# Optimization experiments

Measured on AMD Instinct MI355X. Metric: run time of the kernel, lower is better.

## Reference

```python
import jax, jax.numpy as jnp
import numpy as np

EPS = 1e-5

def _bn(x, gamma, beta):
    # x: [B, N, C]; training-mode BatchNorm1d over (B, N)
    mu = jnp.mean(x, axis=(0, 1))
    var = jnp.var(x, axis=(0, 1))
    return (x - mu) * jax.lax.rsqrt(var + EPS) * gamma + beta


def setup_inputs() -> dict:
    key = jax.random.key(0)
    ks = jax.random.split(key, 32)
    B, N = 16, 8192
    enc_dim, mem_dim = 1024, 1024
    feat_dim = enc_dim + mem_dim  # 2048
    n_points = 2048
    s = 0.02
    d = {
        'partial': jax.random.normal(ks[0], (B, N, 3), jnp.float32),
        # first_conv: Conv1d(3,128,1) + BN(128) + ReLU + Conv1d(128,256,1)
        'W1': jax.random.normal(ks[1], (128, 3), jnp.float32) * s,
        'b1': jnp.zeros((128,), jnp.float32),
        'g1': jnp.ones((128,), jnp.float32),
        'be1': jnp.zeros((128,), jnp.float32),
        'W2': jax.random.normal(ks[2], (256, 128), jnp.float32) * s,
        'b2': jnp.zeros((256,), jnp.float32),
        # second_conv: Conv1d(512,512,1) + BN(512) + ReLU + Conv1d(512,enc_dim,1)
        'W3': jax.random.normal(ks[3], (512, 512), jnp.float32) * s,
        'b3': jnp.zeros((512,), jnp.float32),
        'g2': jnp.ones((512,), jnp.float32),
        'be2': jnp.zeros((512,), jnp.float32),
        'W4': jax.random.normal(ks[4], (enc_dim, 512), jnp.float32) * s,
        'b4': jnp.zeros((enc_dim,), jnp.float32),
        # MemoryModule gates: Linear(enc_dim, mem_dim) x4 + memory param
        'Wf': jax.random.normal(ks[5], (mem_dim, enc_dim), jnp.float32) * s,
        'bf': jnp.zeros((mem_dim,), jnp.float32),
        'Wi': jax.random.normal(ks[6], (mem_dim, enc_dim), jnp.float32) * s,
        'bi': jnp.zeros((mem_dim,), jnp.float32),
        'Wo': jax.random.normal(ks[7], (mem_dim, enc_dim), jnp.float32) * s,
        'bo': jnp.zeros((mem_dim,), jnp.float32),
        'Wc': jax.random.normal(ks[8], (mem_dim, enc_dim), jnp.float32) * s,
        'bc': jnp.zeros((mem_dim,), jnp.float32),
        'mem': jax.random.normal(ks[9], (1, mem_dim), jnp.float32),
        # Decoder MLP: feat_dim->2048->2048->2048->3*n_points
        'D1w': jax.random.normal(ks[10], (2048, feat_dim), jnp.float32) * s,
        'D1b': jnp.zeros((2048,), jnp.float32),
        'D2w': jax.random.normal(ks[11], (2048, 2048), jnp.float32) * s,
        'D2b': jnp.zeros((2048,), jnp.float32),
        'D3w': jax.random.normal(ks[12], (2048, 2048), jnp.float32) * s,
        'D3b': jnp.zeros((2048,), jnp.float32),
        'D4w': jax.random.normal(ks[13], (3 * n_points, 2048), jnp.float32) * s,
        'D4b': jnp.zeros((3 * n_points,), jnp.float32),
    }
    return d


def reference(partial, W1, b1, g1, be1, W2, b2, W3, b3, g2, be2, W4, b4,
              Wf, bf, Wi, bi, Wo, bo, Wc, bc, mem,
              D1w, D1b, D2w, D2b, D3w, D3b, D4w, D4b):
    B, N, _ = partial.shape
    # --- Encoder first_conv (pointwise convs == per-point linear) ---
    f = jnp.einsum('bnc,dc->bnd', partial, W1) + b1          # [B,N,128]
    f = jax.nn.relu(_bn(f, g1, be1))
    f = jnp.einsum('bnc,dc->bnd', f, W2) + b2                # [B,N,256]
    fg = jnp.max(f, axis=1, keepdims=True)                   # [B,1,256]
    f = jnp.concatenate([jnp.broadcast_to(fg, (B, N, 256)), f], axis=-1)  # [B,N,512]
    # --- second_conv ---
    f = jnp.einsum('bnc,dc->bnd', f, W3) + b3                # [B,N,512]
    f = jax.nn.relu(_bn(f, g2, be2))
    f = jnp.einsum('bnc,dc->bnd', f, W4) + b4                # [B,N,enc_dim]
    feat_global = jnp.max(f, axis=1)                         # [B,enc_dim]
    # --- MemoryModule (flag=False: memory not updated) ---
    fgate = jax.nn.sigmoid(feat_global @ Wf.T + bf)
    igate = jax.nn.sigmoid(feat_global @ Wi.T + bi)
    ogate = jax.nn.sigmoid(feat_global @ Wo.T + bo)
    cand = jnp.tanh(feat_global @ Wc.T + bc)
    mem_b = jnp.broadcast_to(mem, fgate.shape)
    h = ogate * jnp.tanh(fgate * mem_b + igate * cand)       # [B,mem_dim]
    feat = jnp.concatenate([feat_global, h], axis=1)         # [B,feat_dim]
    # --- Decoder MLP ---
    z = jax.nn.relu(feat @ D1w.T + D1b)
    z = jax.nn.relu(z @ D2w.T + D2b)
    z = jax.nn.relu(z @ D3w.T + D3b)
    z = z @ D4w.T + D4b                                      # [B, 3*n_points]
    return z.reshape(B, -1, 3)
```

## Files before the change

### kernel.cpp

```cpp
#include <hip/hip_runtime.h>
#include <hip/hip_bf16.h>

typedef __bf16 v8bf __attribute__((ext_vector_type(8)));
typedef float  v4f  __attribute__((ext_vector_type(4)));

#define NPTS (16*8192)
#define RPB  8192

__device__ __forceinline__ unsigned fenc(float x){
    unsigned u = __float_as_uint(x);
    return (u & 0x80000000u) ? ~u : (u | 0x80000000u);
}
__device__ __forceinline__ float fdec(unsigned u){
    return __uint_as_float((u & 0x80000000u) ? (u ^ 0x80000000u) : ~u);
}

__device__ __forceinline__ v8bf bn_relu8(v8bf v, float4 s0, float4 s1, float4 h0, float4 h1){
    v8bf r;
    r[0] = (__bf16)fmaxf(fmaf((float)v[0], s0.x, h0.x), 0.f);
    r[1] = (__bf16)fmaxf(fmaf((float)v[1], s0.y, h0.y), 0.f);
    r[2] = (__bf16)fmaxf(fmaf((float)v[2], s0.z, h0.z), 0.f);
    r[3] = (__bf16)fmaxf(fmaf((float)v[3], s0.w, h0.w), 0.f);
    r[4] = (__bf16)fmaxf(fmaf((float)v[4], s1.x, h1.x), 0.f);
    r[5] = (__bf16)fmaxf(fmaf((float)v[5], s1.y, h1.y), 0.f);
    r[6] = (__bf16)fmaxf(fmaf((float)v[6], s1.z, h1.z), 0.f);
    r[7] = (__bf16)fmaxf(fmaf((float)v[7], s1.w, h1.w), 0.f);
    return r;
}

__global__ __launch_bounds__(256) void stats1_k(const float* __restrict__ P,
        const float* __restrict__ W1, const float* __restrict__ b1,
        float* __restrict__ gsum, float* __restrict__ gsumsq)
{
    int tid = threadIdx.x;
    int c = tid & 127, half = tid >> 7;
    float w0 = W1[c*3+0], w1 = W1[c*3+1], w2 = W1[c*3+2], bb = b1[c];
    float s = 0.f, s2 = 0.f;
    int base = blockIdx.x * 512 + half;
    for (int i = 0; i < 256; ++i) {
        int p = base + i*2;
        float x = P[p*3+0], y = P[p*3+1], z = P[p*3+2];
        float v = fmaf(w0,x, fmaf(w1,y, fmaf(w2,z, bb)));
        s += v; s2 = fmaf(v,v,s2);
    }
    __shared__ float ls[256], lq[256];
    ls[tid] = s; lq[tid] = s2;
    __syncthreads();
    if (half == 0) {
        atomicAdd(&gsum[c],   s  + ls[tid+128]);
        atomicAdd(&gsumsq[c], s2 + lq[tid+128]);
    }
}

__global__ void finalize_k(const float* __restrict__ gsum, const float* __restrict__ gsumsq,
        const float* __restrict__ gamma, const float* __restrict__ beta,
        float* __restrict__ scale, float* __restrict__ shift, int C, float invn)
{
    int c = blockIdx.x*blockDim.x + threadIdx.x;
    if (c >= C) return;
    float m   = gsum[c]*invn;
    float var = fmaxf(gsumsq[c]*invn - m*m, 0.f);
    float rs  = rsqrtf(var + 1e-5f);
    float sc  = gamma[c]*rs;
    scale[c] = sc;
    shift[c] = beta[c] - m*sc;
}

__global__ __launch_bounds__(256) void apply1_k(const float* __restrict__ P,
        const float* __restrict__ W1, const float* __restrict__ b1,
        const float* __restrict__ sc, const float* __restrict__ sh,
        __bf16* __restrict__ out)
{
    int tid = threadIdx.x;
    int c = tid & 127, ph = tid >> 7;
    float w0 = W1[c*3+0], w1 = W1[c*3+1], w2 = W1[c*3+2], bb = b1[c];
    float a = sc[c], b_ = sh[c];
    int base = blockIdx.x * 16 + ph;
    #pragma unroll
    for (int i = 0; i < 8; ++i) {
        int p = base + i*2;
        float x = P[p*3+0], y = P[p*3+1], z = P[p*3+2];
        float v = fmaf(w0,x, fmaf(w1,y, fmaf(w2,z, bb)));
        v = fmaxf(fmaf(v, a, b_), 0.f);
        out[(size_t)p*128 + c] = (__bf16)v;
    }
}

__global__ void cvt_k(const float* __restrict__ src, __bf16* __restrict__ dst,
                      int rows, int cols, int sstride, int coff)
{
    int i = blockIdx.x*256 + threadIdx.x;
    if (i >= rows*cols) return;
    int r = i / cols, c = i - r*cols;
    dst[i] = (__bf16)src[(size_t)r*sstride + coff + c];
}

template<bool STORE, bool DOMAX, bool STATS, bool BNA, int LOGNB>
__global__ __launch_bounds__(256, 2) void gemm_k(
        const __bf16* __restrict__ A, const __bf16* __restrict__ Bw,
        int K, int Nw,
        const float* __restrict__ bias, int bias_bstride,
        __bf16* __restrict__ Cout, unsigned* __restrict__ maxenc,
        float* __restrict__ gsum, float* __restrict__ gsq,
        const float* __restrict__ scA, const float* __restrict__ shA)
{
    __shared__ __bf16 As[128*64];
    __shared__ __bf16 Bs[128*64];
    __shared__ float lstat[2][2][128];

    const int tid  = threadIdx.x;
    const int lane = tid & 63;
    const int wave = tid >> 6;
    const int wr = wave >> 1, wc = wave & 1;

    const int nwg   = (int)gridDim.x;
    const int chunk = nwg >> 3;
    const int bi    = (int)blockIdx.x;
    const int li    = (bi & 7) * chunk + (bi >> 3);
    const int m0    = (li >> LOGNB) * 128;
    const int n0    = (li & ((1 << LOGNB) - 1)) * 128;

    const int srow = tid >> 3, sslot = tid & 7;

    v4f acc[4][4];
    #pragma unroll
    for (int i=0;i<4;i++)
      #pragma unroll
      for (int j=0;j<4;j++) acc[i][j] = (v4f)(0.0f);

    v8bf ra[4], rb[4];
    auto loadAB = [&](int kb){
        float4 s0{}, s1{}, h0{}, h1{};
        if constexpr (BNA) {
            int kk = kb + sslot*8;
            s0 = *(const float4*)(scA + kk);
            s1 = *(const float4*)(scA + kk + 4);
            h0 = *(const float4*)(shA + kk);
            h1 = *(const float4*)(shA + kk + 4);
        }
        #pragma unroll
        for (int i=0;i<4;i++){
            int r = i*32 + srow;
            v8bf v = *(const v8bf*)(A + (size_t)(m0+r)*K + kb + sslot*8);
            if constexpr (BNA) v = bn_relu8(v, s0, s1, h0, h1);
            ra[i] = v;
            rb[i] = *(const v8bf*)(Bw + (size_t)(n0+r)*K + kb + sslot*8);
        }
    };

    loadAB(0);

    for (int k0 = 0; k0 < K; k0 += 64) {
        __syncthreads();
        #pragma unroll
        for (int i=0;i<4;i++){
            int r = i*32 + srow;
            int p = sslot ^ (r & 7);
            *(v8bf*)(&As[r*64 + p*8]) = ra[i];
            *(v8bf*)(&Bs[r*64 + p*8]) = rb[i];
        }
        __syncthreads();
        if (k0 + 64 < K) loadAB(k0 + 64);
        #pragma unroll
        for (int kk = 0; kk < 2; ++kk) {
            v8bf af[4], bfr[4];
            #pragma unroll
            for (int i=0;i<4;i++){
                int arow = wr*64 + i*16 + (lane & 15);
                int slog = kk*4 + (lane >> 4);
                af[i]  = *(const v8bf*)(&As[arow*64 + ((slog ^ (arow & 7))<<3)]);
                int brow = wc*64 + i*16 + (lane & 15);
                bfr[i] = *(const v8bf*)(&Bs[brow*64 + ((slog ^ (brow & 7))<<3)]);
            }
            #pragma unroll
            for (int i=0;i<4;i++)
              #pragma unroll
              for (int j=0;j<4;j++)
                acc[i][j] = __builtin_amdgcn_mfma_f32_16x16x32_bf16(af[i], bfr[j], acc[i][j], 0,0,0);
        }
    }

    const int b = m0 / RPB;
    const float* brow_ = bias + (size_t)b * bias_bstride;
    float colmax[4], csum[4], csq[4];
    #pragma unroll
    for (int j=0;j<4;j++){ colmax[j] = -3.402823466e38f; csum[j]=0.f; csq[j]=0.f; }

    #pragma unroll
    for (int i=0;i<4;i++){
        int rbase = m0 + wr*64 + i*16 + ((lane>>4)<<2);
        #pragma unroll
        for (int j=0;j<4;j++){
            int col = n0 + wc*64 + j*16 + (lane & 15);
            float bv = brow_[col];
            #pragma unroll
            for (int q=0;q<4;q++){
                float v = acc[i][j][q] + bv;
                if constexpr (STORE) Cout[(size_t)(rbase+q)*Nw + col] = (__bf16)v;
                if constexpr (DOMAX) colmax[j] = fmaxf(colmax[j], v);
                if constexpr (STATS) { csum[j] += v; csq[j] = fmaf(v,v,csq[j]); }
            }
        }
    }
    if constexpr (DOMAX) {
        #pragma unroll
        for (int j=0;j<4;j++){
            float v = colmax[j];
            v = fmaxf(v, __shfl_xor(v, 16));
            v = fmaxf(v, __shfl_xor(v, 32));
            if (lane < 16) {
                int col = n0 + wc*64 + j*16 + lane;
                atomicMax(&maxenc[(size_t)b*Nw + col], fenc(v));
            }
        }
    }
    if constexpr (STATS) {
        #pragma unroll
        for (int j=0;j<4;j++){
            float s = csum[j], q = csq[j];
            s += __shfl_xor(s, 16); s += __shfl_xor(s, 32);
            q += __shfl_xor(q, 16); q += __shfl_xor(q, 32);
            if (lane < 16) {
                int c = wc*64 + j*16 + lane;
                lstat[0][wr][c] = s;
                lstat[1][wr][c] = q;
            }
        }
        __syncthreads();
        if (tid < 128) {
            float s = lstat[0][0][tid] + lstat[0][1][tid];
            float q = lstat[1][0][tid] + lstat[1][1][tid];
            atomicAdd(&gsum[n0 + tid], s);
            atomicAdd(&gsq [n0 + tid], q);
        }
    }
}

__global__ __launch_bounds__(256) void bias3_k(const unsigned* __restrict__ fge,
        const float* __restrict__ W3, const float* __restrict__ b3,
        float* __restrict__ bias3)
{
    int b = blockIdx.x, tid = threadIdx.x;
    __shared__ float fg[256];
    fg[tid] = fdec(fge[b*256 + tid]);
    __syncthreads();
    for (int d = tid; d < 512; d += 256) {
        const float* wrow = W3 + (size_t)d*512;
        float s = b3[d];
        for (int c = 0; c < 256; c += 4) {
            s = fmaf(fg[c+0], wrow[c+0], s);
            s = fmaf(fg[c+1], wrow[c+1], s);
            s = fmaf(fg[c+2], wrow[c+2], s);
            s = fmaf(fg[c+3], wrow[c+3], s);
        }
        bias3[b*512 + d] = s;
    }
}

__global__ void decode_k(const unsigned* __restrict__ enc, float* __restrict__ feat)
{
    int i = blockIdx.x*256 + threadIdx.x;
    int b = i >> 10, c = i & 1023;
    feat[(size_t)b*2048 + c] = fdec(enc[i]);
}

__global__ __launch_bounds__(256) void gates_k(
        const float* __restrict__ Wf, const float* __restrict__ bfv,
        const float* __restrict__ Wi, const float* __restrict__ biv,
        const float* __restrict__ Wo, const float* __restrict__ bov,
        const float* __restrict__ Wc, const float* __restrict__ bcv,
        const float* __restrict__ memv, float* __restrict__ feat)
{
    int tid = threadIdx.x;
    int b = tid & 15;
    int j = blockIdx.x*16 + (tid >> 4);
    const float* x  = feat + (size_t)b*2048;
    const float* rf = Wf + (size_t)j*1024;
    const float* ri = Wi + (size_t)j*1024;
    const float* ro = Wo + (size_t)j*1024;
    const float* rc = Wc + (size_t)j*1024;
    float sf = bfv[j], si = biv[j], so = bov[j], scn = bcv[j];
    for (int c = 0; c < 1024; c += 4) {
        float4 xv = *(const float4*)(x + c);
        float4 a  = *(const float4*)(rf + c);
        sf = fmaf(xv.x,a.x, fmaf(xv.y,a.y, fmaf(xv.z,a.z, fmaf(xv.w,a.w, sf))));
        float4 bq = *(const float4*)(ri + c);
        si = fmaf(xv.x,bq.x, fmaf(xv.y,bq.y, fmaf(xv.z,bq.z, fmaf(xv.w,bq.w, si))));
        float4 cq = *(const float4*)(ro + c);
        so = fmaf(xv.x,cq.x, fmaf(xv.y,cq.y, fmaf(xv.z,cq.z, fmaf(xv.w,cq.w, so))));
        float4 dq = *(const float4*)(rc + c);
        scn= fmaf(xv.x,dq.x, fmaf(xv.y,dq.y, fmaf(xv.z,dq.z, fmaf(xv.w,dq.w, scn))));
    }
    float fg = 1.f/(1.f + expf(-sf));
    float ig = 1.f/(1.f + expf(-si));
    float og = 1.f/(1.f + expf(-so));
    float cd = tanhf(scn);
    float h  = og * tanhf(fmaf(fg, memv[j], ig*cd));
    feat[(size_t)b*2048 + 1024 + j] = h;
}

template<bool RELU>
__global__ __launch_bounds__(256) void dec_k(const float* __restrict__ in,
        const float* __restrict__ W, const float* __restrict__ bias,
        float* __restrict__ out, int N)
{
    __shared__ float xin[2048];
    int tid = threadIdx.x;
    int b    = (blockIdx.x*4) / N;
    int col0 = (blockIdx.x*4) % N;
    for (int k = tid; k < 2048; k += 256) xin[k] = in[(size_t)b*2048 + k];
    __syncthreads();
    int lane = tid & 63;
    int col  = col0 + (tid >> 6);
    const float* wrow = W + (size_t)col*2048;
    float s = 0.f;
    for (int k = lane*4; k < 2048; k += 256) {
        float4 wv = *(const float4*)(wrow + k);
        float4 xv = *(const float4*)(&xin[k]);
        s = fmaf(wv.x,xv.x, fmaf(wv.y,xv.y, fmaf(wv.z,xv.z, fmaf(wv.w,xv.w, s))));
    }
    #pragma unroll
    for (int off = 32; off; off >>= 1) s += __shfl_xor(s, off);
    if (lane == 0) {
        s += bias[col];
        if (RELU) s = fmaxf(s, 0.f);
        out[(size_t)b*N + col] = s;
    }
}

extern "C" void kernel_launch(void* const* d_in, const int* in_sizes, int n_in,
                              void* d_out, int out_size, void* d_ws, size_t ws_size,
                              hipStream_t stream)
{
    (void)in_sizes; (void)n_in; (void)out_size; (void)ws_size;
    const float* partial = (const float*)d_in[0];
    const float* W1 = (const float*)d_in[1];
    const float* b1 = (const float*)d_in[2];
    const float* g1 = (const float*)d_in[3];
    const float* be1= (const float*)d_in[4];
    const float* W2 = (const float*)d_in[5];
    const float* b2 = (const float*)d_in[6];
    const float* W3 = (const float*)d_in[7];
    const float* b3 = (const float*)d_in[8];
    const float* g2 = (const float*)d_in[9];
    const float* be2= (const float*)d_in[10];
    const float* W4 = (const float*)d_in[11];
    const float* b4 = (const float*)d_in[12];
    const float* Wf = (const float*)d_in[13];
    const float* bfv= (const float*)d_in[14];
    const float* Wi = (const float*)d_in[15];
    const float* biv= (const float*)d_in[16];
    const float* Wo = (const float*)d_in[17];
    const float* bov= (const float*)d_in[18];
    const float* Wc = (const float*)d_in[19];
    const float* bcv= (const float*)d_in[20];
    const float* memv=(const float*)d_in[21];
    const float* D1w= (const float*)d_in[22];
    const float* D1b= (const float*)d_in[23];
    const float* D2w= (const float*)d_in[24];
    const float* D2b= (const float*)d_in[25];
    const float* D3w= (const float*)d_in[26];
    const float* D3b= (const float*)d_in[27];
    const float* D4w= (const float*)d_in[28];
    const float* D4b= (const float*)d_in[29];

    char* w = (char*)d_ws;
    size_t off = 0;
    auto alloc = [&](size_t bytes) -> void* {
        void* p = w + off; off += (bytes + 255) & ~(size_t)255; return p;
    };
    __bf16* y1bn = (__bf16*)alloc((size_t)NPTS*128*2);
    __bf16* f2   = (__bf16*)alloc((size_t)NPTS*256*2);
    __bf16* y3   = (__bf16*)alloc((size_t)NPTS*512*2);
    __bf16* W2b  = (__bf16*)alloc(256*128*2);
    __bf16* W3bb = (__bf16*)alloc(512*256*2);
    __bf16* W4b  = (__bf16*)alloc(1024*512*2);
    char* accbase = (char*)(w + off);
    float* gsum1    = (float*)alloc(128*4);
    float* gsumsq1  = (float*)alloc(128*4);
    float* gsum3    = (float*)alloc(512*4);
    float* gsumsq3  = (float*)alloc(512*4);
    unsigned* fg_enc    = (unsigned*)alloc(16*256*4);
    unsigned* featg_enc = (unsigned*)alloc(16*1024*4);
    size_t accbytes = (size_t)((w + off) - accbase);
    float* scale1 = (float*)alloc(128*4);
    float* shift1 = (float*)alloc(128*4);
    float* scale3 = (float*)alloc(512*4);
    float* shift3 = (float*)alloc(512*4);
    float* bias3  = (float*)alloc(16*512*4);
    float* feat   = (float*)alloc(16*2048*4);
    float* z1     = (float*)alloc(16*2048*4);
    float* z2     = (float*)alloc(16*2048*4);
    float* z3     = (float*)alloc(16*2048*4);

    hipMemsetAsync(accbase, 0, accbytes, stream);

    cvt_k<<<dim3(128), 256, 0, stream>>>(W2, W2b, 256, 128, 128, 0);
    cvt_k<<<dim3(512), 256, 0, stream>>>(W3, W3bb, 512, 256, 512, 256);
    cvt_k<<<dim3(2048),256, 0, stream>>>(W4, W4b, 1024, 512, 512, 0);

    stats1_k<<<dim3(256), 256, 0, stream>>>(partial, W1, b1, gsum1, gsumsq1);
    finalize_k<<<dim3(1), 128, 0, stream>>>(gsum1, gsumsq1, g1, be1, scale1, shift1, 128, 1.f/NPTS);
    apply1_k<<<dim3(8192), 256, 0, stream>>>(partial, W1, b1, scale1, shift1, y1bn);

    gemm_k<true,true,false,false,1><<<dim3(2048), 256, 0, stream>>>(
        y1bn, W2b, 128, 256, b2, 0, f2, fg_enc, nullptr, nullptr, nullptr, nullptr);

    bias3_k<<<dim3(16), 256, 0, stream>>>(fg_enc, W3, b3, bias3);

    gemm_k<true,false,true,false,2><<<dim3(4096), 256, 0, stream>>>(
        f2, W3bb, 256, 512, bias3, 512, y3, nullptr, gsum3, gsumsq3, nullptr, nullptr);

    finalize_k<<<dim3(2), 256, 0, stream>>>(gsum3, gsumsq3, g2, be2, scale3, shift3, 512, 1.f/NPTS);

    gemm_k<false,true,false,true,3><<<dim3(8192), 256, 0, stream>>>(
        y3, W4b, 512, 1024, b4, 0, nullptr, featg_enc, nullptr, nullptr, scale3, shift3);

    decode_k<<<dim3(64), 256, 0, stream>>>(featg_enc, feat);
    gates_k<<<dim3(64), 256, 0, stream>>>(Wf,bfv, Wi,biv, Wo,bov, Wc,bcv, memv, feat);

    dec_k<true ><<<dim3(8192),  256, 0, stream>>>(feat, D1w, D1b, z1, 2048);
    dec_k<true ><<<dim3(8192),  256, 0, stream>>>(z1,   D2w, D2b, z2, 2048);
    dec_k<true ><<<dim3(8192),  256, 0, stream>>>(z2,   D3w, D3b, z3, 2048);
    dec_k<false><<<dim3(24576), 256, 0, stream>>>(z3,   D4w, D4b, (float*)d_out, 6144);
}
```

Before: 567.7 us.

## Add 256x256-tile 8-wave double-buffered GEMM for the two big pointwise convs

Adds a new GEMM kernel with 256x256 output tiles, 512 threads, a double-buffered LDS stage, phased MFMA issue with s_setprio, and BN scale/shift cached in LDS. It is used for the W3 and W4 convolutions in place of the 128x128 kernel, which raises data reuse per tile and overlaps global loads with compute. The original kernel is trimmed to the plain store/max path for W2. Larger tiles mean fewer workgroups and heavier register and LDS use per workgroup, which may limit occupancy.

```diff
diff --git a/kernel.cpp b/kernel.cpp
--- a/kernel.cpp
+++ b/kernel.cpp
@@ -95,31 +95,25 @@
     dst[i] = (__bf16)src[(size_t)r*sstride + coff + c];
 }
 
-template<bool STORE, bool DOMAX, bool STATS, bool BNA, int LOGNB>
+template<bool STORE, bool DOMAX, int LOGNB>
 __global__ __launch_bounds__(256, 2) void gemm_k(
         const __bf16* __restrict__ A, const __bf16* __restrict__ Bw,
         int K, int Nw,
         const float* __restrict__ bias, int bias_bstride,
-        __bf16* __restrict__ Cout, unsigned* __restrict__ maxenc,
-        float* __restrict__ gsum, float* __restrict__ gsq,
-        const float* __restrict__ scA, const float* __restrict__ shA)
+        __bf16* __restrict__ Cout, unsigned* __restrict__ maxenc)
 {
     __shared__ __bf16 As[128*64];
     __shared__ __bf16 Bs[128*64];
-    __shared__ float lstat[2][2][128];
-
     const int tid  = threadIdx.x;
     const int lane = tid & 63;
     const int wave = tid >> 6;
     const int wr = wave >> 1, wc = wave & 1;
-
     const int nwg   = (int)gridDim.x;
     const int chunk = nwg >> 3;
     const int bi    = (int)blockIdx.x;
     const int li    = (bi & 7) * chunk + (bi >> 3);
     const int m0    = (li >> LOGNB) * 128;
     const int n0    = (li & ((1 << LOGNB) - 1)) * 128;
-
     const int srow = tid >> 3, sslot = tid & 7;
 
     v4f acc[4][4];
@@ -129,26 +123,12 @@
       for (int j=0;j<4;j++) acc[i][j] = (v4f)(0.0f);
 
     v8bf ra[4], rb[4];
-    auto loadAB = [&](int kb){
-        float4 s0{}, s1{}, h0{}, h1{};
-        if constexpr (BNA) {
-            int kk = kb + sslot*8;
-            s0 = *(const float4*)(scA + kk);
-            s1 = *(const float4*)(scA + kk + 4);
-            h0 = *(const float4*)(shA + kk);
-            h1 = *(const float4*)(shA + kk + 4);
-        }
-        #pragma unroll
-        for (int i=0;i<4;i++){
-            int r = i*32 + srow;
-            v8bf v = *(const v8bf*)(A + (size_t)(m0+r)*K + kb + sslot*8);
-            if constexpr (BNA) v = bn_relu8(v, s0, s1, h0, h1);
-            ra[i] = v;
-            rb[i] = *(const v8bf*)(Bw + (size_t)(n0+r)*K + kb + sslot*8);
-        }
-    };
-
-    loadAB(0);
+    #pragma unroll
+    for (int i=0;i<4;i++){
+        int r = i*32 + srow;
+        ra[i] = *(const v8bf*)(A  + (size_t)(m0+r)*K + sslot*8);
+        rb[i] = *(const v8bf*)(Bw + (size_t)(n0+r)*K + sslot*8);
+    }
 
     for (int k0 = 0; k0 < K; k0 += 64) {
         __syncthreads();
@@ -160,7 +140,14 @@
             *(v8bf*)(&Bs[r*64 + p*8]) = rb[i];
         }
         __syncthreads();
-        if (k0 + 64 < K) loadAB(k0 + 64);
+        if (k0 + 64 < K) {
+            #pragma unroll
+            for (int i=0;i<4;i++){
+                int r = i*32 + srow;
+                ra[i] = *(const v8bf*)(A  + (size_t)(m0+r)*K + (k0+64) + sslot*8);
+                rb[i] = *(const v8bf*)(Bw + (size_t)(n0+r)*K + (k0+64) + sslot*8);
+            }
+        }
         #pragma unroll
         for (int kk = 0; kk < 2; ++kk) {
             v8bf af[4], bfr[4];
@@ -182,9 +169,9 @@
 
     const int b = m0 / RPB;
     const float* brow_ = bias + (size_t)b * bias_bstride;
-    float colmax[4], csum[4], csq[4];
-    #pragma unroll
-    for (int j=0;j<4;j++){ colmax[j] = -3.402823466e38f; csum[j]=0.f; csq[j]=0.f; }
+    float colmax[4];
+    #pragma unroll
+    for (int j=0;j<4;j++) colmax[j] = -3.402823466e38f;
 
     #pragma unroll
     for (int i=0;i<4;i++){
@@ -198,7 +185,6 @@
                 float v = acc[i][j][q] + bv;
                 if constexpr (STORE) Cout[(size_t)(rbase+q)*Nw + col] = (__bf16)v;
                 if constexpr (DOMAX) colmax[j] = fmaxf(colmax[j], v);
-                if constexpr (STATS) { csum[j] += v; csq[j] = fmaf(v,v,csq[j]); }
             }
         }
     }
@@ -214,7 +200,169 @@
             }
         }
     }
+}
+
+template<bool STORE, bool DOMAX, bool STATS, bool BNA, int LOGNB>
+__global__ __launch_bounds__(512, 2) void gemm8_k(
+        const __bf16* __restrict__ A, const __bf16* __restrict__ Bw,
+        int K, int Nw,
+        const float* __restrict__ bias, int bias_bstride,
+        __bf16* __restrict__ Cout, unsigned* __restrict__ maxenc,
+        float* __restrict__ gsum, float* __restrict__ gsq,
+        const float* __restrict__ scA, const float* __restrict__ shA)
+{
+    __shared__ __bf16 lds[2][2][256*64];
+    __shared__ float bnbuf[2][512];
+
+    const int tid  = threadIdx.x;
+    const int lane = tid & 63;
+    const int wave = tid >> 6;
+    const int wr = wave >> 2, wc = wave & 3;
+    const int nwg   = (int)gridDim.x;
+    const int chunk = nwg >> 3;
+    const int bi    = (int)blockIdx.x;
+    const int li    = (bi & 7) * chunk + (bi >> 3);
+    const int m0    = (li >> LOGNB) * 256;
+    const int n0    = (li & ((1 << LOGNB) - 1)) * 256;
+    const int srow = tid >> 3;
+    const int slot = tid & 7;
+
+    if constexpr (BNA) {
+        for (int c = tid; c < K; c += 512) {
+            bnbuf[0][c] = scA[c];
+            bnbuf[1][c] = shA[c];
+        }
+    }
+
+    v4f acc[8][4];
+    #pragma unroll
+    for (int i=0;i<8;i++)
+      #pragma unroll
+      for (int j=0;j<4;j++) acc[i][j] = (v4f)(0.0f);
+
+    v8bf ga[4], gb[4];
+    auto issue = [&](int kb){
+        #pragma unroll
+        for (int p=0;p<4;p++){
+            int r = p*64 + srow;
+            ga[p] = *(const v8bf*)(A  + (size_t)(m0+r)*K + kb + slot*8);
+            gb[p] = *(const v8bf*)(Bw + (size_t)(n0+r)*K + kb + slot*8);
+        }
+    };
+    auto wr_lds = [&](int buf, int kb){
+        float4 s0{}, s1{}, h0{}, h1{};
+        if constexpr (BNA) {
+            int kk = kb + slot*8;
+            s0 = *(const float4*)&bnbuf[0][kk];
+            s1 = *(const float4*)&bnbuf[0][kk+4];
+            h0 = *(const float4*)&bnbuf[1][kk];
+            h1 = *(const float4*)&bnbuf[1][kk+4];
+        }
+        #pragma unroll
+        for (int p=0;p<4;p++){
+            int r = p*64 + srow;
+            int sl = slot ^ (r & 7);
+            v8bf va = ga[p];
+            if constexpr (BNA) va = bn_relu8(va, s0, s1, h0, h1);
+            *(v8bf*)(&lds[buf][0][r*64 + sl*8]) = va;
+            *(v8bf*)(&lds[buf][1][r*64 + sl*8]) = gb[p];
+        }
+    };
+
+    if constexpr (BNA) __syncthreads();
+    issue(0);
+    wr_lds(0, 0);
+    issue(64);
+    __syncthreads();
+
+    const int nt = K >> 6;
+    for (int t = 0; t < nt; ++t) {
+        const __bf16* as_ = &lds[t & 1][0][0];
+        const __bf16* bs_ = &lds[t & 1][1][0];
+        v8bf bfr[4][2];
+        #pragma unroll
+        for (int ph = 0; ph < 4; ++ph) {
+            v8bf af[2][2];
+            if (ph == 0) {
+                #pragma unroll
+                for (int nf=0;nf<4;nf++)
+                  #pragma unroll
+                  for (int kk=0;kk<2;kk++){
+                    int brow = wc*64 + nf*16 + (lane & 15);
+                    int sg = kk*4 + (lane >> 4);
+                    bfr[nf][kk] = *(const v8bf*)(bs_ + brow*64 + ((sg ^ (brow & 7))<<3));
+                  }
+            }
+            #pragma unroll
+            for (int i=0;i<2;i++)
+              #pragma unroll
+              for (int kk=0;kk<2;kk++){
+                int arow = wr*128 + (ph*2+i)*16 + (lane & 15);
+                int sg = kk*4 + (lane >> 4);
+                af[i][kk] = *(const v8bf*)(as_ + arow*64 + ((sg ^ (arow & 7))<<3));
+              }
+            __builtin_amdgcn_s_barrier();
+            asm volatile("s_waitcnt lgkmcnt(0)" ::: "memory");
+            __builtin_amdgcn_sched_barrier(0);
+            __builtin_amdgcn_s_setprio(1);
+            #pragma unroll
+            for (int i=0;i<2;i++)
+              #pragma unroll
+              for (int nf=0;nf<4;nf++)
+                acc[ph*2+i][nf] = __builtin_amdgcn_mfma_f32_16x16x32_bf16(af[i][0], bfr[nf][0], acc[ph*2+i][nf], 0,0,0);
+            #pragma unroll
+            for (int i=0;i<2;i++)
+              #pragma unroll
+              for (int nf=0;nf<4;nf++)
+                acc[ph*2+i][nf] = __builtin_amdgcn_mfma_f32_16x16x32_bf16(af[i][1], bfr[nf][1], acc[ph*2+i][nf], 0,0,0);
+            __builtin_amdgcn_s_setprio(0);
+            if (ph < 3) {
+                __builtin_amdgcn_s_barrier();
+            } else {
+                __syncthreads();
+                if (t + 1 < nt) wr_lds((t+1) & 1, (t+1) << 6);
+                if (t + 2 < nt) issue((t+2) << 6);
+                __syncthreads();
+            }
+        }
+    }
+
+    const int b = m0 / RPB;
+    const float* brow_ = bias + (size_t)b * bias_bstride;
+    float colmax[4], csum[4], csq[4];
+    #pragma unroll
+    for (int j=0;j<4;j++){ colmax[j] = -3.402823466e38f; csum[j]=0.f; csq[j]=0.f; }
+
+    #pragma unroll
+    for (int i=0;i<8;i++){
+        int rbase = m0 + wr*128 + i*16 + ((lane>>4)<<2);
+        #pragma unroll
+        for (int j=0;j<4;j++){
+            int col = n0 + wc*64 + j*16 + (lane & 15);
+            float bv = brow_[col];
+            #pragma unroll
+            for (int q=0;q<4;q++){
+                float v = acc[i][j][q] + bv;
+                if constexpr (STORE) Cout[(size_t)(rbase+q)*Nw + col] = (__bf16)v;
+                if constexpr (DOMAX) colmax[j] = fmaxf(colmax[j], v);
+                if constexpr (STATS) { csum[j] += v; csq[j] = fmaf(v,v,csq[j]); }
+            }
+        }
+    }
+    if constexpr (DOMAX) {
+        #pragma unroll
+        for (int j=0;j<4;j++){
+            float v = colmax[j];
+            v = fmaxf(v, __shfl_xor(v, 16));
+            v = fmaxf(v, __shfl_xor(v, 32));
+            if (lane < 16) {
+                int col = n0 + wc*64 + j*16 + lane;
+                atomicMax(&maxenc[(size_t)b*Nw + col], fenc(v));
+            }
+        }
+    }
     if constexpr (STATS) {
+        float* lst = (float*)&lds[0][0][0];
         #pragma unroll
         for (int j=0;j<4;j++){
             float s = csum[j], q = csq[j];
@@ -222,14 +370,14 @@
             q += __shfl_xor(q, 16); q += __shfl_xor(q, 32);
             if (lane < 16) {
                 int c = wc*64 + j*16 + lane;
-                lstat[0][wr][c] = s;
-                lstat[1][wr][c] = q;
+                lst[(wr*2+0)*256 + c] = s;
+                lst[(wr*2+1)*256 + c] = q;
             }
         }
         __syncthreads();
-        if (tid < 128) {
-            float s = lstat[0][0][tid] + lstat[0][1][tid];
-            float q = lstat[1][0][tid] + lstat[1][1][tid];
+        if (tid < 256) {
+            float s = lst[0*256 + tid] + lst[2*256 + tid];
+            float q = lst[1*256 + tid] + lst[3*256 + tid];
             atomicAdd(&gsum[n0 + tid], s);
             atomicAdd(&gsq [n0 + tid], q);
         }
@@ -403,17 +551,17 @@
     finalize_k<<<dim3(1), 128, 0, stream>>>(gsum1, gsumsq1, g1, be1, scale1, shift1, 128, 1.f/NPTS);
     apply1_k<<<dim3(8192), 256, 0, stream>>>(partial, W1, b1, scale1, shift1, y1bn);
 
-    gemm_k<true,true,false,false,1><<<dim3(2048), 256, 0, stream>>>(
-        y1bn, W2b, 128, 256, b2, 0, f2, fg_enc, nullptr, nullptr, nullptr, nullptr);
+    gemm_k<true,true,1><<<dim3(2048), 256, 0, stream>>>(
+        y1bn, W2b, 128, 256, b2, 0, f2, fg_enc);
 
     bias3_k<<<dim3(16), 256, 0, stream>>>(fg_enc, W3, b3, bias3);
 
-    gemm_k<true,false,true,false,2><<<dim3(4096), 256, 0, stream>>>(
+    gemm8_k<true,false,true,false,1><<<dim3(1024), 512, 0, stream>>>(
         f2, W3bb, 256, 512, bias3, 512, y3, nullptr, gsum3, gsumsq3, nullptr, nullptr);
 
     finalize_k<<<dim3(2), 256, 0, stream>>>(gsum3, gsumsq3, g2, be2, scale3, shift3, 512, 1.f/NPTS);
 
-    gemm_k<false,true,false,true,3><<<dim3(8192), 256, 0, stream>>>(
+    gemm8_k<false,true,false,true,2><<<dim3(2048), 512, 0, stream>>>(
         y3, W4b, 512, 1024, b4, 0, nullptr, featg_enc, nullptr, nullptr, scale3, shift3);
 
     decode_k<<<dim3(64), 256, 0, stream>>>(featg_enc, feat);
```

Result: no change. 574.2 us (+1.1%).

## Batch decoder GEMV across all 16 samples to reuse each weight row

Applied to the files above, without the earlier changes.

The decoder MLP kernels previously read every weight row once per batch sample, so weights were fetched 16 times. The new kernel loads all 16 input vectors into shared memory (128KB) and has each wave compute two output columns for all batch rows, reading each weight row once. This cuts global weight traffic about sixteenfold. The cost is far fewer blocks (256 or 768), heavy shared-memory use that limits occupancy, and 16 accumulators per lane.

```diff
diff --git a/kernel.cpp b/kernel.cpp
--- a/kernel.cpp
+++ b/kernel.cpp
@@ -112,14 +112,12 @@
     const int lane = tid & 63;
     const int wave = tid >> 6;
     const int wr = wave >> 1, wc = wave & 1;
-
     const int nwg   = (int)gridDim.x;
     const int chunk = nwg >> 3;
     const int bi    = (int)blockIdx.x;
     const int li    = (bi & 7) * chunk + (bi >> 3);
     const int m0    = (li >> LOGNB) * 128;
     const int n0    = (li & ((1 << LOGNB) - 1)) * 128;
-
     const int srow = tid >> 3, sslot = tid & 7;
 
     v4f acc[4][4];
@@ -300,31 +298,47 @@
 }
 
 template<bool RELU>
-__global__ __launch_bounds__(256) void dec_k(const float* __restrict__ in,
+__global__ __launch_bounds__(256) void dec2_k(const float* __restrict__ in,
         const float* __restrict__ W, const float* __restrict__ bias,
         float* __restrict__ out, int N)
 {
-    __shared__ float xin[2048];
+    __shared__ float xin[16*2048];
     int tid = threadIdx.x;
-    int b    = (blockIdx.x*4) / N;
-    int col0 = (blockIdx.x*4) % N;
-    for (int k = tid; k < 2048; k += 256) xin[k] = in[(size_t)b*2048 + k];
+    for (int i = tid; i < 8192; i += 256)
+        *(float4*)&xin[i*4] = *(const float4*)&in[i*4];
     __syncthreads();
-    int lane = tid & 63;
-    int col  = col0 + (tid >> 6);
-    const float* wrow = W + (size_t)col*2048;
-    float s = 0.f;
-    for (int k = lane*4; k < 2048; k += 256) {
-        float4 wv = *(const float4*)(wrow + k);
-        float4 xv = *(const float4*)(&xin[k]);
-        s = fmaf(wv.x,xv.x, fmaf(wv.y,xv.y, fmaf(wv.z,xv.z, fmaf(wv.w,xv.w, s))));
-    }
+    int lane = tid & 63, wv = tid >> 6;
     #pragma unroll
-    for (int off = 32; off; off >>= 1) s += __shfl_xor(s, off);
-    if (lane == 0) {
-        s += bias[col];
-        if (RELU) s = fmaxf(s, 0.f);
-        out[(size_t)b*N + col] = s;
+    for (int c = 0; c < 2; ++c) {
+        int col = blockIdx.x*8 + wv*2 + c;
+        const float* wrow = W + (size_t)col*2048;
+        float s[16];
+        #pragma unroll
+        for (int b=0;b<16;b++) s[b]=0.f;
+        #pragma unroll
+        for (int it = 0; it < 8; ++it) {
+            int k = it*256 + lane*4;
+            float4 w4 = *(const float4*)(wrow + k);
+            #pragma unroll
+            for (int b=0;b<16;b++){
+                const float* xb = &xin[b*2048 + k];
+                s[b] = fmaf(w4.x, xb[0], fmaf(w4.y, xb[1], fmaf(w4.z, xb[2], fmaf(w4.w, xb[3], s[b]))));
+            }
+        }
+        #pragma unroll
+        for (int off=32; off; off>>=1){
+            #pragma unroll
+            for (int b=0;b<16;b++) s[b] += __shfl_xor(s[b], off);
+        }
+        if (lane == 0) {
+            float bv = bias[col];
+            #pragma unroll
+            for (int b=0;b<16;b++){
+                float v = s[b] + bv;
+                if (RELU) v = fmaxf(v, 0.f);
+                out[(size_t)b*N + col] = v;
+            }
+        }
     }
 }
 
@@ -419,8 +433,8 @@
     decode_k<<<dim3(64), 256, 0, stream>>>(featg_enc, feat);
     gates_k<<<dim3(64), 256, 0, stream>>>(Wf,bfv, Wi,biv, Wo,bov, Wc,bcv, memv, feat);
 
-    dec_k<true ><<<dim3(8192),  256, 0, stream>>>(feat, D1w, D1b, z1, 2048);
-    dec_k<true ><<<dim3(8192),  256, 0, stream>>>(z1,   D2w, D2b, z2, 2048);
-    dec_k<true ><<<dim3(8192),  256, 0, stream>>>(z2,   D3w, D3b, z3, 2048);
-    dec_k<false><<<dim3(24576), 256, 0, stream>>>(z3,   D4w, D4b, (float*)d_out, 6144);
-}
+    dec2_k<true ><<<dim3(256), 256, 0, stream>>>(feat, D1w, D1b, z1, 2048);
+    dec2_k<true ><<<dim3(256), 256, 0, stream>>>(z1,   D2w, D2b, z2, 2048);
+    dec2_k<true ><<<dim3(256), 256, 0, stream>>>(z2,   D3w, D3b, z3, 2048);
+    dec2_k<false><<<dim3(768), 256, 0, stream>>>(z3,   D4w, D4b, (float*)d_out, 6144);
+}
```

Result: faster. 507.4 us (-10.6%).
